# Kernel tuning notes

Measured on AMD Instinct MI355X. Metric: run time of the kernel, lower is better.

The kernel has to match this reference:

```python
import jax, jax.numpy as jnp
import numpy as np

EMBED_DIM = 1024
NUM_HEADS = 16
HEAD_DIM = EMBED_DIM // NUM_HEADS
B, T = 4, 2048


def setup_inputs() -> dict:
    key = jax.random.key(0)
    ks = jax.random.split(key, 5)
    s = 1.0 / np.sqrt(EMBED_DIM)
    x = jax.random.normal(ks[0], (B, T, EMBED_DIM), dtype=jnp.float32)
    W_qkv = jax.random.uniform(ks[1], (EMBED_DIM, 3 * EMBED_DIM), minval=-s, maxval=s, dtype=jnp.float32)
    b_qkv = jax.random.uniform(ks[2], (3 * EMBED_DIM,), minval=-s, maxval=s, dtype=jnp.float32)
    W_proj = jax.random.uniform(ks[3], (EMBED_DIM, EMBED_DIM), minval=-s, maxval=s, dtype=jnp.float32)
    b_proj = jax.random.uniform(ks[4], (EMBED_DIM,), minval=-s, maxval=s, dtype=jnp.float32)
    return {"x": x, "W_qkv": W_qkv, "b_qkv": b_qkv, "W_proj": W_proj, "b_proj": b_proj}


def reference(x, W_qkv, b_qkv, W_proj, b_proj):
    Bq, Tq, C = x.shape
    H, D = NUM_HEADS, HEAD_DIM
    qkv = x @ W_qkv + b_qkv                      # [B,T,3C]
    qkv = qkv.reshape(Bq, Tq, 3, H, D)
    q = qkv[:, :, 0].transpose(0, 2, 1, 3)       # [B,H,T,D]
    k = qkv[:, :, 1].transpose(0, 2, 1, 3)
    v = qkv[:, :, 2].transpose(0, 2, 1, 3)
    scale = 1.0 / jnp.sqrt(jnp.asarray(D, x.dtype))
    attn = jnp.einsum('bhqd,bhkd->bhqk', q, k) * scale  # [B,H,T,T]
    mask = jnp.tril(jnp.ones((Tq, Tq), dtype=bool))     # causal: keep lower triangle
    attn = jnp.where(mask, attn, jnp.asarray(-jnp.inf, attn.dtype))
    attn = jax.nn.softmax(attn, axis=-1)
    out = jnp.einsum('bhqk,bhkd->bhqd', attn, v)        # [B,H,T,D]
    out = out.transpose(0, 2, 1, 3).reshape(Bq, Tq, C)
    return out @ W_proj + b_proj
```

## Files before the change

### kernel.cpp

```cpp
#include <hip/hip_runtime.h>
#include <stdint.h>

typedef unsigned short ushort_t;
typedef __attribute__((ext_vector_type(4))) unsigned int  u32x4;
typedef __attribute__((ext_vector_type(2))) unsigned int  u32x2;
typedef __attribute__((ext_vector_type(4))) float         f32x4;
typedef __attribute__((ext_vector_type(8))) __bf16        bf16x8;
typedef __attribute__((ext_vector_type(2))) __bf16        bf16x2;

__device__ __forceinline__ ushort_t f2bf(float f) {
    unsigned int u = __float_as_uint(f);
    u += 0x7fffu + ((u >> 16) & 1u);
    return (ushort_t)(u >> 16);
}
__device__ __forceinline__ unsigned int pack2bf(float a, float b) {
    return (unsigned int)f2bf(a) | ((unsigned int)f2bf(b) << 16);
}
#if __has_builtin(__builtin_amdgcn_cvt_pk_bf16_f32)
__device__ __forceinline__ unsigned int pack2bf_fast(float a, float b) {
    bf16x2 v = __builtin_amdgcn_cvt_pk_bf16_f32(a, b);
    return __builtin_bit_cast(unsigned int, v);
}
#else
__device__ __forceinline__ unsigned int pack2bf_fast(float a, float b) {
    return pack2bf(a, b);
}
#endif
__device__ __forceinline__ f32x4 mfma16(bf16x8 a, bf16x8 b, f32x4 c) {
    return __builtin_amdgcn_mfma_f32_16x16x32_bf16(a, b, c, 0, 0, 0);
}
__device__ __forceinline__ bf16x8 ldfrag(const ushort_t* p) {
    return __builtin_bit_cast(bf16x8, *(const u32x4*)p);
}

#define QSCALE 0.18033688011112042f

__global__ __launch_bounds__(256) void xcast(const float* __restrict__ X,
                                             ushort_t* __restrict__ Xb) {
    long i = ((long)blockIdx.x * 256 + threadIdx.x) * 8;
    float4 a = *(const float4*)(X + i);
    float4 b = *(const float4*)(X + i + 4);
    u32x4 pk;
    pk.x = pack2bf(a.x, a.y); pk.y = pack2bf(a.z, a.w);
    pk.z = pack2bf(b.x, b.y); pk.w = pack2bf(b.z, b.w);
    *(u32x4*)(Xb + i) = pk;
}

__global__ __launch_bounds__(256) void wt_kernel(const float* __restrict__ W,
                                                 ushort_t* __restrict__ Wt,
                                                 int K, int N) {
    __shared__ float tile[32][33];
    int tx = threadIdx.x, ty = threadIdx.y;
    int n0 = blockIdx.x * 32, k0 = blockIdx.y * 32;
    for (int p = 0; p < 4; ++p)
        tile[ty + 8*p][tx] = W[(long)(k0 + ty + 8*p) * N + n0 + tx];
    __syncthreads();
    for (int p = 0; p < 4; ++p)
        Wt[(long)(n0 + ty + 8*p) * K + k0 + tx] = f2bf(tile[tx][ty + 8*p]);
}

__global__ __launch_bounds__(256) void gemm_qkv(const ushort_t* __restrict__ Xb,
                                                const ushort_t* __restrict__ Wt,
                                                const float* __restrict__ bias,
                                                ushort_t* __restrict__ Qo,
                                                ushort_t* __restrict__ Ko,
                                                ushort_t* __restrict__ Vto) {
    __shared__ __align__(16) ushort_t smem[128 * 136];

    const int tid  = threadIdx.x;
    const int g    = blockIdx.x;
    const int grp  = g / 192, rr = g % 192;
    const int m0   = (grp * 8 + (rr & 7)) * 128;
    const int n0   = (rr >> 3) * 128;
    const int lane = tid & 63, w = tid >> 6;
    const int quad = lane >> 4, l16 = lane & 15;
    const int wm = (w >> 1) * 64, wn = (w & 1) * 64;

    const int srow  = tid >> 2;
    const int slot  = tid & 3;
    const int oct   = slot ^ ((tid >> 3) & 3);
    const int wofs  = srow * 32 + slot * 8;
    const int rslot = (quad ^ ((l16 >> 1) & 3)) * 8;

    const ushort_t* Ap = Xb + (long)(m0 + srow) * 1024 + oct * 8;
    const ushort_t* Bp = Wt + (long)(n0 + srow) * 1024 + oct * 8;

    f32x4 acc[4][4] = {};

    u32x4 Ag0 = *(const u32x4*)(Ap);
    u32x4 Ag1 = *(const u32x4*)(Ap + 65536);
    u32x4 Bg0 = *(const u32x4*)(Bp);
    u32x4 Bg1 = *(const u32x4*)(Bp + 65536);

    for (int k0 = 0; k0 < 1024; k0 += 32) {
        int kn = (k0 + 32 < 1024) ? k0 + 32 : k0;
        u32x4 An0 = *(const u32x4*)(Ap + kn);
        u32x4 An1 = *(const u32x4*)(Ap + kn + 65536);
        u32x4 Bn0 = *(const u32x4*)(Bp + kn);
        u32x4 Bn1 = *(const u32x4*)(Bp + kn + 65536);

        ushort_t* As = smem + ((k0 >> 5) & 1) * 4096;
        ushort_t* Bs = smem + 8192 + ((k0 >> 5) & 1) * 4096;
        *(u32x4*)&As[wofs]        = Ag0;
        *(u32x4*)&As[wofs + 2048] = Ag1;
        *(u32x4*)&Bs[wofs]        = Bg0;
        *(u32x4*)&Bs[wofs + 2048] = Bg1;
        __syncthreads();

        bf16x8 af[4], bfr[4];
        for (int i = 0; i < 4; ++i)
            af[i] = ldfrag(&As[(wm + 16*i + l16) * 32 + rslot]);
        for (int j = 0; j < 4; ++j)
            bfr[j] = ldfrag(&Bs[(wn + 16*j + l16) * 32 + rslot]);
        for (int i = 0; i < 4; ++i)
            for (int j = 0; j < 4; ++j)
                acc[i][j] = mfma16(af[i], bfr[j], acc[i][j]);

        Ag0 = An0; Ag1 = An1; Bg0 = Bn0; Bg1 = Bn1;
    }

    float bj[4];
    for (int j = 0; j < 4; ++j) bj[j] = bias[n0 + wn + 16*j + l16];
    const int bb = m0 >> 11, t0m = m0 & 2047;
    __syncthreads();

    if (n0 < 2048) {
        ushort_t* dst = (n0 < 1024) ? Qo : Ko;
        const float scale = (n0 < 1024) ? QSCALE : 1.0f;
        const int nbase = (n0 < 1024) ? n0 : n0 - 1024;
        for (int i = 0; i < 4; ++i)
            for (int j = 0; j < 4; ++j) {
                int nl = wn + 16*j + l16;
                for (int r = 0; r < 4; ++r) {
                    int ml = wm + 16*i + quad*4 + r;
                    smem[ml * 136 + nl] = f2bf((acc[i][j][r] + bj[j]) * scale);
                }
            }
        __syncthreads();
        for (int c = 0; c < 8; ++c) {
            int chunk = tid + 256 * c;
            int row = chunk >> 4, nc = (chunk & 15) * 8;
            int n = nbase + nc;
            int hh = n >> 6, d = n & 63;
            *(u32x4*)&dst[((long)(bb*16 + hh) * 2048 + t0m + row) * 64 + d] =
                *(const u32x4*)&smem[row * 136 + nc];
        }
    } else {
        for (int i = 0; i < 4; ++i)
            for (int j = 0; j < 4; ++j) {
                int nl = wn + 16*j + l16;
                for (int r = 0; r < 4; ++r) {
                    int ml = wm + 16*i + quad*4 + r;
                    smem[nl * 136 + ml] = f2bf(acc[i][j][r] + bj[j]);
                }
            }
        __syncthreads();
        for (int c = 0; c < 8; ++c) {
            int chunk = tid + 256 * c;
            int row = chunk >> 4, mc = (chunk & 15) * 8;
            int n = n0 - 2048 + row;
            int hh = n >> 6, d = n & 63;
            *(u32x4*)&Vto[((long)(bb*16 + hh) * 64 + d) * 2048 + t0m + mc] =
                *(const u32x4*)&smem[row * 136 + mc];
        }
    }
}

__global__ __launch_bounds__(256) void attn_kernel(const ushort_t* __restrict__ Q,
                                                   const ushort_t* __restrict__ K,
                                                   const ushort_t* __restrict__ Vt,
                                                   ushort_t* __restrict__ O) {
    __shared__ __align__(16) ushort_t Ks[2][64 * 64];
    __shared__ __align__(16) ushort_t Vs[2][64 * 64];
    __shared__ __align__(16) ushort_t Ps[128 * 72];

    const int tid  = threadIdx.x;
    const int lane = tid & 63, w = tid >> 6, quad = lane >> 4, l16 = lane & 15;
    const int p    = blockIdx.x & 7;
    const int bh   = blockIdx.x >> 3;
    const ushort_t* qptr = Q  + (long)bh * 2048 * 64;
    const ushort_t* kptr = K  + (long)bh * 2048 * 64;
    const ushort_t* vptr = Vt + (long)bh * 64 * 2048;
    const int bb2 = bh >> 4, h = bh & 15;

    const int srow = tid >> 3;
    const int slot = tid & 7;
    const int oct  = slot ^ (srow & 7);
    const int koff = srow * 64 + oct * 8;
    const int voff = srow * 2048 + oct * 8;
    const int wofs = srow * 64 + slot * 8;

    for (int ti = 0; ti < 2; ++ti) {
        const int qt = ti ? (15 - p) : p;
        const int qbase = qt * 128;
        const int nkt = 2 * qt + 2;

        __syncthreads();
        for (int c = 0; c < 4; ++c) {
            int flat = tid + 256 * c;
            int row = flat >> 3, kc = (flat & 7) * 8;
            *(u32x4*)&Ps[row * 72 + kc] = *(const u32x4*)&qptr[(long)(qbase + row) * 64 + kc];
        }
        __syncthreads();
        bf16x8 qf[2][2];
        for (int nt = 0; nt < 2; ++nt)
            for (int kk = 0; kk < 2; ++kk)
                qf[nt][kk] = ldfrag(&Ps[(32*w + 16*nt + l16) * 72 + kk*32 + quad*8]);

        f32x4 acc[2][4] = {};
        float l_run[2] = {0.f, 0.f};

        u32x4 Kg0 = *(const u32x4*)(kptr + koff);
        u32x4 Kg1 = *(const u32x4*)(kptr + koff + 2048);
        u32x4 Vg0 = *(const u32x4*)(vptr + voff);
        u32x4 Vg1 = *(const u32x4*)(vptr + voff + 65536);

        for (int kt = 0; kt < nkt; ++kt) {
            const int kbase = kt * 64;
            const int kn = (kt + 1 < nkt) ? kt + 1 : kt;
            u32x4 Kn0 = *(const u32x4*)(kptr + kn*4096 + koff);
            u32x4 Kn1 = *(const u32x4*)(kptr + kn*4096 + koff + 2048);
            u32x4 Vn0 = *(const u32x4*)(vptr + kn*64 + voff);
            u32x4 Vn1 = *(const u32x4*)(vptr + kn*64 + voff + 65536);

            ushort_t* Kb = Ks[kt & 1];
            ushort_t* Vb = Vs[kt & 1];
            *(u32x4*)&Kb[wofs]        = Kg0;
            *(u32x4*)&Kb[wofs + 2048] = Kg1;
            *(u32x4*)&Vb[wofs]        = Vg0;
            *(u32x4*)&Vb[wofs + 2048] = Vg1;
            __syncthreads();

            if (kbase <= qbase + 32*w + 31) {
                f32x4 s[4][2] = {};
                for (int kk = 0; kk < 2; ++kk)
                    for (int mt = 0; mt < 4; ++mt) {
                        bf16x8 kf = ldfrag(&Kb[(16*mt + l16) * 64 + ((4*kk + quad) ^ (l16 & 7)) * 8]);
                        for (int nt = 0; nt < 2; ++nt)
                            s[mt][nt] = mfma16(kf, qf[nt][kk], s[mt][nt]);
                    }
                if (kbase + 63 > qbase + 32*w) {
                    for (int mt = 0; mt < 4; ++mt)
                        for (int nt = 0; nt < 2; ++nt) {
                            int qv = qbase + 32*w + 16*nt + l16;
                            for (int r = 0; r < 4; ++r)
                                if (kbase + 16*mt + 4*quad + r > qv)
                                    s[mt][nt][r] = -__builtin_inff();
                        }
                }
                for (int nt = 0; nt < 2; ++nt)
                    for (int mt = 0; mt < 4; ++mt) {
                        float p0 = __builtin_amdgcn_exp2f(s[mt][nt][0]);
                        float p1 = __builtin_amdgcn_exp2f(s[mt][nt][1]);
                        float p2 = __builtin_amdgcn_exp2f(s[mt][nt][2]);
                        float p3 = __builtin_amdgcn_exp2f(s[mt][nt][3]);
                        l_run[nt] += (p0 + p1) + (p2 + p3);
                        u32x2 pk;
                        pk.x = pack2bf_fast(p0, p1);
                        pk.y = pack2bf_fast(p2, p3);
                        *(u32x2*)&Ps[(32*w + 16*nt + l16) * 72 + 16*mt + 4*quad] = pk;
                    }
                for (int kk = 0; kk < 2; ++kk) {
                    bf16x8 pf0 = ldfrag(&Ps[(32*w + l16) * 72 + kk*32 + quad*8]);
                    bf16x8 pf1 = ldfrag(&Ps[(32*w + 16 + l16) * 72 + kk*32 + quad*8]);
                    for (int jd = 0; jd < 4; ++jd) {
                        bf16x8 vf = ldfrag(&Vb[(16*jd + l16) * 64 + ((4*kk + quad) ^ (l16 & 7)) * 8]);
                        acc[0][jd] = mfma16(pf0, vf, acc[0][jd]);
                        acc[1][jd] = mfma16(pf1, vf, acc[1][jd]);
                    }
                }
            }
            Kg0 = Kn0; Kg1 = Kn1; Vg0 = Vn0; Vg1 = Vn1;
        }

        for (int i = 0; i < 2; ++i) {
            float l = l_run[i];
            l += __shfl_xor(l, 16, 64);
            l += __shfl_xor(l, 32, 64);
            for (int r = 0; r < 4; ++r) {
                float linv = 1.0f / __shfl(l, (lane & 48) | (4*quad + r), 64);
                int t = qbase + 32*w + 16*i + 4*quad + r;
                for (int jd = 0; jd < 4; ++jd) {
                    int d = 16*jd + l16;
                    O[((long)(bb2*2048 + t)) * 1024 + h*64 + d] = f2bf(acc[i][jd][r] * linv);
                }
            }
        }
    }
}

__global__ __launch_bounds__(256) void gemm_proj(const ushort_t* __restrict__ A,
                                                 const ushort_t* __restrict__ Wt,
                                                 const float* __restrict__ bias,
                                                 float* __restrict__ Out) {
    __shared__ __align__(16) ushort_t smem[4 * 4096];

    const int tid  = threadIdx.x;
    const int g    = blockIdx.x;
    const int grp  = g / 64, rr = g % 64;
    const int m0   = (grp * 8 + (rr & 7)) * 128;
    const int n0   = (rr >> 3) * 128;
    const int lane = tid & 63, w = tid >> 6;
    const int quad = lane >> 4, l16 = lane & 15;
    const int wm = (w >> 1) * 64, wn = (w & 1) * 64;

    const int srow  = tid >> 2;
    const int slot  = tid & 3;
    const int oct   = slot ^ ((tid >> 3) & 3);
    const int wofs  = srow * 32 + slot * 8;
    const int rslot = (quad ^ ((l16 >> 1) & 3)) * 8;

    const ushort_t* Ap = A  + (long)(m0 + srow) * 1024 + oct * 8;
    const ushort_t* Bp = Wt + (long)(n0 + srow) * 1024 + oct * 8;

    f32x4 acc[4][4] = {};

    u32x4 Ag0 = *(const u32x4*)(Ap);
    u32x4 Ag1 = *(const u32x4*)(Ap + 65536);
    u32x4 Bg0 = *(const u32x4*)(Bp);
    u32x4 Bg1 = *(const u32x4*)(Bp + 65536);

    for (int k0 = 0; k0 < 1024; k0 += 32) {
        int kn = (k0 + 32 < 1024) ? k0 + 32 : k0;
        u32x4 An0 = *(const u32x4*)(Ap + kn);
        u32x4 An1 = *(const u32x4*)(Ap + kn + 65536);
        u32x4 Bn0 = *(const u32x4*)(Bp + kn);
        u32x4 Bn1 = *(const u32x4*)(Bp + kn + 65536);

        ushort_t* As = smem + ((k0 >> 5) & 1) * 4096;
        ushort_t* Bs = smem + 8192 + ((k0 >> 5) & 1) * 4096;
        *(u32x4*)&As[wofs]        = Ag0;
        *(u32x4*)&As[wofs + 2048] = Ag1;
        *(u32x4*)&Bs[wofs]        = Bg0;
        *(u32x4*)&Bs[wofs + 2048] = Bg1;
        __syncthreads();

        bf16x8 af[4], bfr[4];
        for (int i = 0; i < 4; ++i)
            af[i] = ldfrag(&As[(wm + 16*i + l16) * 32 + rslot]);
        for (int j = 0; j < 4; ++j)
            bfr[j] = ldfrag(&Bs[(wn + 16*j + l16) * 32 + rslot]);
        for (int i = 0; i < 4; ++i)
            for (int j = 0; j < 4; ++j)
                acc[i][j] = mfma16(af[i], bfr[j], acc[i][j]);

        Ag0 = An0; Ag1 = An1; Bg0 = Bn0; Bg1 = Bn1;
    }

    float bj[4];
    for (int j = 0; j < 4; ++j) bj[j] = bias[n0 + wn + 16*j + l16];
    for (int i = 0; i < 4; ++i)
        for (int j = 0; j < 4; ++j)
            for (int r = 0; r < 4; ++r) {
                int m = m0 + wm + 16*i + quad*4 + r;
                int n = n0 + wn + 16*j + l16;
                Out[(long)m * 1024 + n] = acc[i][j][r] + bj[j];
            }
}

extern "C" void kernel_launch(void* const* d_in, const int* in_sizes, int n_in,
                              void* d_out, int out_size, void* d_ws, size_t ws_size,
                              hipStream_t stream) {
    const float* x     = (const float*)d_in[0];
    const float* Wqkv  = (const float*)d_in[1];
    const float* bqkv  = (const float*)d_in[2];
    const float* Wproj = (const float*)d_in[3];
    const float* bproj = (const float*)d_in[4];
    float* out = (float*)d_out;

    ushort_t* wqkvt  = (ushort_t*)d_ws;
    ushort_t* wprojt = wqkvt  + 3072 * 1024;
    ushort_t* Qb     = wprojt + 1024 * 1024;
    ushort_t* Kb     = Qb  + 8388608;
    ushort_t* Vtb    = Kb  + 8388608;
    ushort_t* XbA2   = Vtb + 8388608;

    xcast<<<4096, 256, 0, stream>>>(x, XbA2);
    wt_kernel<<<dim3(96, 32), dim3(32, 8), 0, stream>>>(Wqkv, wqkvt, 1024, 3072);
    wt_kernel<<<dim3(32, 32), dim3(32, 8), 0, stream>>>(Wproj, wprojt, 1024, 1024);
    gemm_qkv<<<1536, 256, 0, stream>>>(XbA2, wqkvt, bqkv, Qb, Kb, Vtb);
    attn_kernel<<<512, 256, 0, stream>>>(Qb, Kb, Vtb, XbA2);
    gemm_proj<<<512, 256, 0, stream>>>(XbA2, wprojt, bproj, out);
}
```

Baseline: 258.7 us.

## Deepen global prefetch to two stages and remap attention block order

The QKV GEMM, the output projection GEMM and the attention kernel switch from a one-stage register prefetch to two register sets feeding alternating LDS buffers. Each global load is now issued two tiles ahead, giving it more time to complete before the data is needed. The attention grid mapping also changes so consecutive blocks cover different batch-heads with the same query-tile pair, which may change load balance and L2 locality. The cost is more live registers, which may lower occupancy, and the attention loop assumes an even tile count (nkt = 2*qt+2, which always holds).

Measured after the change: 244.7 us. -5.4%, faster.

```diff
diff --git a/kernel.cpp b/kernel.cpp
--- a/kernel.cpp
+++ b/kernel.cpp
@@ -87,36 +87,60 @@
 
     f32x4 acc[4][4] = {};
 
-    u32x4 Ag0 = *(const u32x4*)(Ap);
-    u32x4 Ag1 = *(const u32x4*)(Ap + 65536);
-    u32x4 Bg0 = *(const u32x4*)(Bp);
-    u32x4 Bg1 = *(const u32x4*)(Bp + 65536);
-
-    for (int k0 = 0; k0 < 1024; k0 += 32) {
-        int kn = (k0 + 32 < 1024) ? k0 + 32 : k0;
-        u32x4 An0 = *(const u32x4*)(Ap + kn);
-        u32x4 An1 = *(const u32x4*)(Ap + kn + 65536);
-        u32x4 Bn0 = *(const u32x4*)(Bp + kn);
-        u32x4 Bn1 = *(const u32x4*)(Bp + kn + 65536);
-
-        ushort_t* As = smem + ((k0 >> 5) & 1) * 4096;
-        ushort_t* Bs = smem + 8192 + ((k0 >> 5) & 1) * 4096;
-        *(u32x4*)&As[wofs]        = Ag0;
-        *(u32x4*)&As[wofs + 2048] = Ag1;
-        *(u32x4*)&Bs[wofs]        = Bg0;
-        *(u32x4*)&Bs[wofs + 2048] = Bg1;
-        __syncthreads();
-
-        bf16x8 af[4], bfr[4];
-        for (int i = 0; i < 4; ++i)
-            af[i] = ldfrag(&As[(wm + 16*i + l16) * 32 + rslot]);
-        for (int j = 0; j < 4; ++j)
-            bfr[j] = ldfrag(&Bs[(wn + 16*j + l16) * 32 + rslot]);
-        for (int i = 0; i < 4; ++i)
+    u32x4 AA0 = *(const u32x4*)(Ap);
+    u32x4 AA1 = *(const u32x4*)(Ap + 65536);
+    u32x4 BA0 = *(const u32x4*)(Bp);
+    u32x4 BA1 = *(const u32x4*)(Bp + 65536);
+    u32x4 AB0 = *(const u32x4*)(Ap + 32);
+    u32x4 AB1 = *(const u32x4*)(Ap + 32 + 65536);
+    u32x4 BB0 = *(const u32x4*)(Bp + 32);
+    u32x4 BB1 = *(const u32x4*)(Bp + 32 + 65536);
+
+    for (int k0 = 0; k0 < 1024; k0 += 64) {
+        {
+            ushort_t* As = smem;
+            ushort_t* Bs = smem + 8192;
+            *(u32x4*)&As[wofs]        = AA0;
+            *(u32x4*)&As[wofs + 2048] = AA1;
+            *(u32x4*)&Bs[wofs]        = BA0;
+            *(u32x4*)&Bs[wofs + 2048] = BA1;
+            int kf = (k0 + 64 < 1024) ? k0 + 64 : k0;
+            AA0 = *(const u32x4*)(Ap + kf);
+            AA1 = *(const u32x4*)(Ap + kf + 65536);
+            BA0 = *(const u32x4*)(Bp + kf);
+            BA1 = *(const u32x4*)(Bp + kf + 65536);
+            __syncthreads();
+            bf16x8 af[4], bfr[4];
+            for (int i = 0; i < 4; ++i)
+                af[i] = ldfrag(&As[(wm + 16*i + l16) * 32 + rslot]);
             for (int j = 0; j < 4; ++j)
-                acc[i][j] = mfma16(af[i], bfr[j], acc[i][j]);
-
-        Ag0 = An0; Ag1 = An1; Bg0 = Bn0; Bg1 = Bn1;
+                bfr[j] = ldfrag(&Bs[(wn + 16*j + l16) * 32 + rslot]);
+            for (int i = 0; i < 4; ++i)
+                for (int j = 0; j < 4; ++j)
+                    acc[i][j] = mfma16(af[i], bfr[j], acc[i][j]);
+        }
+        {
+            ushort_t* As = smem + 4096;
+            ushort_t* Bs = smem + 8192 + 4096;
+            *(u32x4*)&As[wofs]        = AB0;
+            *(u32x4*)&As[wofs + 2048] = AB1;
+            *(u32x4*)&Bs[wofs]        = BB0;
+            *(u32x4*)&Bs[wofs + 2048] = BB1;
+            int kf = (k0 + 96 < 1024) ? k0 + 96 : k0 + 32;
+            AB0 = *(const u32x4*)(Ap + kf);
+            AB1 = *(const u32x4*)(Ap + kf + 65536);
+            BB0 = *(const u32x4*)(Bp + kf);
+            BB1 = *(const u32x4*)(Bp + kf + 65536);
+            __syncthreads();
+            bf16x8 af[4], bfr[4];
+            for (int i = 0; i < 4; ++i)
+                af[i] = ldfrag(&As[(wm + 16*i + l16) * 32 + rslot]);
+            for (int j = 0; j < 4; ++j)
+                bfr[j] = ldfrag(&Bs[(wn + 16*j + l16) * 32 + rslot]);
+            for (int i = 0; i < 4; ++i)
+                for (int j = 0; j < 4; ++j)
+                    acc[i][j] = mfma16(af[i], bfr[j], acc[i][j]);
+        }
     }
 
     float bj[4];
@@ -176,8 +200,9 @@
 
     const int tid  = threadIdx.x;
     const int lane = tid & 63, w = tid >> 6, quad = lane >> 4, l16 = lane & 15;
-    const int p    = blockIdx.x & 7;
-    const int bh   = blockIdx.x >> 3;
+    const int g    = blockIdx.x;
+    const int bh   = (g & 7) + 8 * ((g >> 3) & 7);
+    const int p    = g >> 6;
     const ushort_t* qptr = Q  + (long)bh * 2048 * 64;
     const ushort_t* kptr = K  + (long)bh * 2048 * 64;
     const ushort_t* vptr = Vt + (long)bh * 64 * 2048;
@@ -210,67 +235,84 @@
         f32x4 acc[2][4] = {};
         float l_run[2] = {0.f, 0.f};
 
-        u32x4 Kg0 = *(const u32x4*)(kptr + koff);
-        u32x4 Kg1 = *(const u32x4*)(kptr + koff + 2048);
-        u32x4 Vg0 = *(const u32x4*)(vptr + voff);
-        u32x4 Vg1 = *(const u32x4*)(vptr + voff + 65536);
-
-        for (int kt = 0; kt < nkt; ++kt) {
+        auto phase = [&](int kt, ushort_t* Kb, ushort_t* Vb) {
             const int kbase = kt * 64;
-            const int kn = (kt + 1 < nkt) ? kt + 1 : kt;
-            u32x4 Kn0 = *(const u32x4*)(kptr + kn*4096 + koff);
-            u32x4 Kn1 = *(const u32x4*)(kptr + kn*4096 + koff + 2048);
-            u32x4 Vn0 = *(const u32x4*)(vptr + kn*64 + voff);
-            u32x4 Vn1 = *(const u32x4*)(vptr + kn*64 + voff + 65536);
-
-            ushort_t* Kb = Ks[kt & 1];
-            ushort_t* Vb = Vs[kt & 1];
-            *(u32x4*)&Kb[wofs]        = Kg0;
-            *(u32x4*)&Kb[wofs + 2048] = Kg1;
-            *(u32x4*)&Vb[wofs]        = Vg0;
-            *(u32x4*)&Vb[wofs + 2048] = Vg1;
-            __syncthreads();
-
-            if (kbase <= qbase + 32*w + 31) {
-                f32x4 s[4][2] = {};
-                for (int kk = 0; kk < 2; ++kk)
-                    for (int mt = 0; mt < 4; ++mt) {
-                        bf16x8 kf = ldfrag(&Kb[(16*mt + l16) * 64 + ((4*kk + quad) ^ (l16 & 7)) * 8]);
-                        for (int nt = 0; nt < 2; ++nt)
-                            s[mt][nt] = mfma16(kf, qf[nt][kk], s[mt][nt]);
+            if (kbase > qbase + 32*w + 31) return;
+            f32x4 s[4][2] = {};
+            for (int kk = 0; kk < 2; ++kk)
+                for (int mt = 0; mt < 4; ++mt) {
+                    bf16x8 kf = ldfrag(&Kb[(16*mt + l16) * 64 + ((4*kk + quad) ^ (l16 & 7)) * 8]);
+                    for (int nt = 0; nt < 2; ++nt)
+                        s[mt][nt] = mfma16(kf, qf[nt][kk], s[mt][nt]);
+                }
+            if (kbase + 63 > qbase + 32*w) {
+                for (int mt = 0; mt < 4; ++mt)
+                    for (int nt = 0; nt < 2; ++nt) {
+                        int qv = qbase + 32*w + 16*nt + l16;
+                        for (int r = 0; r < 4; ++r)
+                            if (kbase + 16*mt + 4*quad + r > qv)
+                                s[mt][nt][r] = -__builtin_inff();
                     }
-                if (kbase + 63 > qbase + 32*w) {
-                    for (int mt = 0; mt < 4; ++mt)
-                        for (int nt = 0; nt < 2; ++nt) {
-                            int qv = qbase + 32*w + 16*nt + l16;
-                            for (int r = 0; r < 4; ++r)
-                                if (kbase + 16*mt + 4*quad + r > qv)
-                                    s[mt][nt][r] = -__builtin_inff();
-                        }
-                }
-                for (int nt = 0; nt < 2; ++nt)
-                    for (int mt = 0; mt < 4; ++mt) {
-                        float p0 = __builtin_amdgcn_exp2f(s[mt][nt][0]);
-                        float p1 = __builtin_amdgcn_exp2f(s[mt][nt][1]);
-                        float p2 = __builtin_amdgcn_exp2f(s[mt][nt][2]);
-                        float p3 = __builtin_amdgcn_exp2f(s[mt][nt][3]);
-                        l_run[nt] += (p0 + p1) + (p2 + p3);
-                        u32x2 pk;
-                        pk.x = pack2bf_fast(p0, p1);
-                        pk.y = pack2bf_fast(p2, p3);
-                        *(u32x2*)&Ps[(32*w + 16*nt + l16) * 72 + 16*mt + 4*quad] = pk;
-                    }
-                for (int kk = 0; kk < 2; ++kk) {
-                    bf16x8 pf0 = ldfrag(&Ps[(32*w + l16) * 72 + kk*32 + quad*8]);
-                    bf16x8 pf1 = ldfrag(&Ps[(32*w + 16 + l16) * 72 + kk*32 + quad*8]);
-                    for (int jd = 0; jd < 4; ++jd) {
-                        bf16x8 vf = ldfrag(&Vb[(16*jd + l16) * 64 + ((4*kk + quad) ^ (l16 & 7)) * 8]);
-                        acc[0][jd] = mfma16(pf0, vf, acc[0][jd]);
-                        acc[1][jd] = mfma16(pf1, vf, acc[1][jd]);
-                    }
-                }
-            }
-            Kg0 = Kn0; Kg1 = Kn1; Vg0 = Vn0; Vg1 = Vn1;
+            }
+            for (int nt = 0; nt < 2; ++nt)
+                for (int mt = 0; mt < 4; ++mt) {
+                    float p0 = __builtin_amdgcn_exp2f(s[mt][nt][0]);
+                    float p1 = __builtin_amdgcn_exp2f(s[mt][nt][1]);
+                    float p2 = __builtin_amdgcn_exp2f(s[mt][nt][2]);
+                    float p3 = __builtin_amdgcn_exp2f(s[mt][nt][3]);
+                    l_run[nt] += (p0 + p1) + (p2 + p3);
+                    u32x2 pk;
+                    pk.x = pack2bf_fast(p0, p1);
+                    pk.y = pack2bf_fast(p2, p3);
+                    *(u32x2*)&Ps[(32*w + 16*nt + l16) * 72 + 16*mt + 4*quad] = pk;
+                }
+            for (int kk = 0; kk < 2; ++kk) {
+                bf16x8 pf0 = ldfrag(&Ps[(32*w + l16) * 72 + kk*32 + quad*8]);
+                bf16x8 pf1 = ldfrag(&Ps[(32*w + 16 + l16) * 72 + kk*32 + quad*8]);
+                for (int jd = 0; jd < 4; ++jd) {
+                    bf16x8 vf = ldfrag(&Vb[(16*jd + l16) * 64 + ((4*kk + quad) ^ (l16 & 7)) * 8]);
+                    acc[0][jd] = mfma16(pf0, vf, acc[0][jd]);
+                    acc[1][jd] = mfma16(pf1, vf, acc[1][jd]);
+                }
+            }
+        };
+
+        u32x4 KA0 = *(const u32x4*)(kptr + koff);
+        u32x4 KA1 = *(const u32x4*)(kptr + koff + 2048);
+        u32x4 VA0 = *(const u32x4*)(vptr + voff);
+        u32x4 VA1 = *(const u32x4*)(vptr + voff + 65536);
+        u32x4 KB0 = *(const u32x4*)(kptr + 4096 + koff);
+        u32x4 KB1 = *(const u32x4*)(kptr + 4096 + koff + 2048);
+        u32x4 VB0 = *(const u32x4*)(vptr + 64 + voff);
+        u32x4 VB1 = *(const u32x4*)(vptr + 64 + voff + 65536);
+
+        for (int kt = 0; kt < nkt; kt += 2) {
+            {
+                *(u32x4*)&Ks[0][wofs]        = KA0;
+                *(u32x4*)&Ks[0][wofs + 2048] = KA1;
+                *(u32x4*)&Vs[0][wofs]        = VA0;
+                *(u32x4*)&Vs[0][wofs + 2048] = VA1;
+                int kf = (kt + 2 < nkt) ? kt + 2 : kt;
+                KA0 = *(const u32x4*)(kptr + kf*4096 + koff);
+                KA1 = *(const u32x4*)(kptr + kf*4096 + koff + 2048);
+                VA0 = *(const u32x4*)(vptr + kf*64 + voff);
+                VA1 = *(const u32x4*)(vptr + kf*64 + voff + 65536);
+                __syncthreads();
+                phase(kt, Ks[0], Vs[0]);
+            }
+            {
+                *(u32x4*)&Ks[1][wofs]        = KB0;
+                *(u32x4*)&Ks[1][wofs + 2048] = KB1;
+                *(u32x4*)&Vs[1][wofs]        = VB0;
+                *(u32x4*)&Vs[1][wofs + 2048] = VB1;
+                int kf = (kt + 3 < nkt) ? kt + 3 : kt + 1;
+                KB0 = *(const u32x4*)(kptr + kf*4096 + koff);
+                KB1 = *(const u32x4*)(kptr + kf*4096 + koff + 2048);
+                VB0 = *(const u32x4*)(vptr + kf*64 + voff);
+                VB1 = *(const u32x4*)(vptr + kf*64 + voff + 65536);
+                __syncthreads();
+                phase(kt + 1, Ks[1], Vs[1]);
+            }
         }
 
         for (int i = 0; i < 2; ++i) {
@@ -315,36 +357,60 @@
 
     f32x4 acc[4][4] = {};
 
-    u32x4 Ag0 = *(const u32x4*)(Ap);
-    u32x4 Ag1 = *(const u32x4*)(Ap + 65536);
-    u32x4 Bg0 = *(const u32x4*)(Bp);
-    u32x4 Bg1 = *(const u32x4*)(Bp + 65536);
-
-    for (int k0 = 0; k0 < 1024; k0 += 32) {
-        int kn = (k0 + 32 < 1024) ? k0 + 32 : k0;
-        u32x4 An0 = *(const u32x4*)(Ap + kn);
-        u32x4 An1 = *(const u32x4*)(Ap + kn + 65536);
-        u32x4 Bn0 = *(const u32x4*)(Bp + kn);
-        u32x4 Bn1 = *(const u32x4*)(Bp + kn + 65536);
-
-        ushort_t* As = smem + ((k0 >> 5) & 1) * 4096;
-        ushort_t* Bs = smem + 8192 + ((k0 >> 5) & 1) * 4096;
-        *(u32x4*)&As[wofs]        = Ag0;
-        *(u32x4*)&As[wofs + 2048] = Ag1;
-        *(u32x4*)&Bs[wofs]        = Bg0;
-        *(u32x4*)&Bs[wofs + 2048] = Bg1;
-        __syncthreads();
-
-        bf16x8 af[4], bfr[4];
-        for (int i = 0; i < 4; ++i)
-            af[i] = ldfrag(&As[(wm + 16*i + l16) * 32 + rslot]);
-        for (int j = 0; j < 4; ++j)
-            bfr[j] = ldfrag(&Bs[(wn + 16*j + l16) * 32 + rslot]);
-        for (int i = 0; i < 4; ++i)
+    u32x4 AA0 = *(const u32x4*)(Ap);
+    u32x4 AA1 = *(const u32x4*)(Ap + 65536);
+    u32x4 BA0 = *(const u32x4*)(Bp);
+    u32x4 BA1 = *(const u32x4*)(Bp + 65536);
+    u32x4 AB0 = *(const u32x4*)(Ap + 32);
+    u32x4 AB1 = *(const u32x4*)(Ap + 32 + 65536);
+    u32x4 BB0 = *(const u32x4*)(Bp + 32);
+    u32x4 BB1 = *(const u32x4*)(Bp + 32 + 65536);
+
+    for (int k0 = 0; k0 < 1024; k0 += 64) {
+        {
+            ushort_t* As = smem;
+            ushort_t* Bs = smem + 8192;
+            *(u32x4*)&As[wofs]        = AA0;
+            *(u32x4*)&As[wofs + 2048] = AA1;
+            *(u32x4*)&Bs[wofs]        = BA0;
+            *(u32x4*)&Bs[wofs + 2048] = BA1;
+            int kf = (k0 + 64 < 1024) ? k0 + 64 : k0;
+            AA0 = *(const u32x4*)(Ap + kf);
+            AA1 = *(const u32x4*)(Ap + kf + 65536);
+            BA0 = *(const u32x4*)(Bp + kf);
+            BA1 = *(const u32x4*)(Bp + kf + 65536);
+            __syncthreads();
+            bf16x8 af[4], bfr[4];
+            for (int i = 0; i < 4; ++i)
+                af[i] = ldfrag(&As[(wm + 16*i + l16) * 32 + rslot]);
             for (int j = 0; j < 4; ++j)
-                acc[i][j] = mfma16(af[i], bfr[j], acc[i][j]);
-
-        Ag0 = An0; Ag1 = An1; Bg0 = Bn0; Bg1 = Bn1;
+                bfr[j] = ldfrag(&Bs[(wn + 16*j + l16) * 32 + rslot]);
+            for (int i = 0; i < 4; ++i)
+                for (int j = 0; j < 4; ++j)
+                    acc[i][j] = mfma16(af[i], bfr[j], acc[i][j]);
+        }
+        {
+            ushort_t* As = smem + 4096;
+            ushort_t* Bs = smem + 8192 + 4096;
+            *(u32x4*)&As[wofs]        = AB0;
+            *(u32x4*)&As[wofs + 2048] = AB1;
+            *(u32x4*)&Bs[wofs]        = BB0;
+            *(u32x4*)&Bs[wofs + 2048] = BB1;
+            int kf = (k0 + 96 < 1024) ? k0 + 96 : k0 + 32;
+            AB0 = *(const u32x4*)(Ap + kf);
+            AB1 = *(const u32x4*)(Ap + kf + 65536);
+            BB0 = *(const u32x4*)(Bp + kf);
+            BB1 = *(const u32x4*)(Bp + kf + 65536);
+            __syncthreads();
+            bf16x8 af[4], bfr[4];
+            for (int i = 0; i < 4; ++i)
+                af[i] = ldfrag(&As[(wm + 16*i + l16) * 32 + rslot]);
+            for (int j = 0; j < 4; ++j)
+                bfr[j] = ldfrag(&Bs[(wn + 16*j + l16) * 32 + rslot]);
+            for (int i = 0; i < 4; ++i)
+                for (int j = 0; j < 4; ++j)
+                    acc[i][j] = mfma16(af[i], bfr[j], acc[i][j]);
+        }
     }
 
     float bj[4];
```
